# Kernel tuning notes

Hardware: AMD Instinct MI355X
Metric: run time of the kernel (lower is better)

## Reference

```python
import jax, jax.numpy as jnp
import numpy as np

NUM_HEADS = 16
LN_EPS = 1e-5


def _rope(x):
    """lucidrains RotaryEmbedding(dim_per_head // 2): rotate only the first
    Dh//2 channels with interleaved pairs; pass the rest through.
    x: (B, H, S, Dh)"""
    S, D = x.shape[-2], x.shape[-1]
    rot = D // 2
    inv_freq = 1.0 / (10000.0 ** (jnp.arange(0, rot, 2, dtype=jnp.float32) / rot))  # (rot//2,)
    ang = jnp.arange(S, dtype=jnp.float32)[:, None] * inv_freq[None, :]             # (S, rot//2)
    ang = jnp.repeat(ang, 2, axis=-1)                                               # (S, rot)
    cos, sin = jnp.cos(ang), jnp.sin(ang)
    xr, xp = x[..., :rot], x[..., rot:]
    x1, x2 = xr[..., 0::2], xr[..., 1::2]
    rot_half = jnp.stack((-x2, x1), axis=-1).reshape(xr.shape)  # interleaved (-x2, x1)
    xr = xr * cos + rot_half * sin
    return jnp.concatenate([xr, xp], axis=-1)


def setup_inputs() -> dict:
    key = jax.random.key(0)
    k1, k2, k3 = jax.random.split(key, 3)
    B, S, D = 4, 2048, 2048
    X = jax.random.normal(k1, (B, S, D), dtype=jnp.float32)
    ln_w = jnp.ones((D,), dtype=jnp.float32)
    ln_b = jnp.zeros((D,), dtype=jnp.float32)
    W_in = jax.random.normal(k2, (D, 3 * D), dtype=jnp.float32) * 0.02
    W_out = jax.random.normal(k3, (D, D), dtype=jnp.float32) * 0.02
    return {"X": X, "ln_w": ln_w, "ln_b": ln_b, "W_in": W_in, "W_out": W_out}


def reference(X, ln_w, ln_b, W_in, W_out):
    B, S, D = X.shape
    H = NUM_HEADS
    Dh = D // H
    # pre-norm (LayerNorm)
    mu = jnp.mean(X, axis=-1, keepdims=True)
    var = jnp.mean(jnp.square(X - mu), axis=-1, keepdims=True)
    Xn = (X - mu) * jax.lax.rsqrt(var + LN_EPS) * ln_w + ln_b
    # fused QKV projection
    qkv = jnp.einsum('bsd,df->bsf', Xn, W_in)            # (B, S, 3D)
    Q, K, V = jnp.split(qkv, 3, axis=-1)
    Q = Q.reshape(B, S, H, Dh).transpose(0, 2, 1, 3)     # (B, H, S, Dh)
    K = K.reshape(B, S, H, Dh).transpose(0, 2, 1, 3)
    V = V.reshape(B, S, H, Dh).transpose(0, 2, 1, 3)
    Q, K = _rope(Q), _rope(K)
    scores = jnp.einsum('bhqd,bhkd->bhqk', Q, K) / jnp.sqrt(jnp.float32(Dh))
    probs = jax.nn.softmax(scores, axis=-1)              # acausal: no mask
    ctx = jnp.einsum('bhqk,bhkd->bhqd', probs, V)
    ctx = ctx.transpose(0, 2, 1, 3).reshape(B, S, D)
    out = jnp.einsum('bsd,df->bsf', ctx, W_out)
    return out + X
```

## Files before the change

### kernel.cpp

```cpp
#include <hip/hip_runtime.h>
#include <hip/hip_bf16.h>
#include <cstddef>

#define B_ 4
#define S_ 2048
#define D_ 2048
#define H_ 16
#define DH_ 128
#define QKS_ 4096

typedef __attribute__((ext_vector_type(8))) short bfrag8;
typedef __attribute__((ext_vector_type(4))) float ffrag4;
typedef __attribute__((ext_vector_type(4))) int ifrag4;

typedef const __attribute__((address_space(1))) void* gptr1;
typedef __attribute__((address_space(3))) void* lptr3;
#define GL16(g, l) __builtin_amdgcn_global_load_lds((gptr1)(g), (lptr3)(l), 16, 0, 0)
#define LDSU(p) ((unsigned)(unsigned long long)(lptr3)(p))

#define BARRIER() { asm volatile("" ::: "memory"); __builtin_amdgcn_s_barrier(); asm volatile("" ::: "memory"); }
#define VMW8() asm volatile("s_waitcnt vmcnt(8)" ::: "memory")
#define VMW6() asm volatile("s_waitcnt vmcnt(6)" ::: "memory")
#define VMW4() asm volatile("s_waitcnt vmcnt(4)" ::: "memory")
#define VMW0() asm volatile("s_waitcnt vmcnt(0)" ::: "memory")
#define LGKM(n) { asm volatile("s_waitcnt lgkmcnt(" #n ")" ::: "memory"); __builtin_amdgcn_sched_barrier(0); }

__device__ __forceinline__ bfrag8 DSR128(unsigned a) {
  ifrag4 r;
  asm volatile("ds_read_b128 %0, %1" : "=v"(r) : "v"(a));
  return __builtin_bit_cast(bfrag8, r);
}

__device__ __forceinline__ short f2bf(float f) {
  unsigned u = __float_as_uint(f);
  u = (u + 0x7FFFu + ((u >> 16) & 1u)) >> 16;
  return (short)u;
}
__device__ __forceinline__ float bf2f(short s) {
  return __uint_as_float(((unsigned)(unsigned short)s) << 16);
}
__device__ __forceinline__ unsigned cvtpk(float lo, float hi) {
  unsigned r;
  asm("v_cvt_pk_bf16_f32 %0, %1, %2" : "=v"(r) : "v"(lo), "v"(hi));
  return r;
}

__global__ __launch_bounds__(256) void rope_tab_kernel(float2* __restrict__ tab) {
  int idx = blockIdx.x * 256 + threadIdx.x;
  int s = idx >> 5, p = idx & 31;
  float invf = exp2f(-(float)p * (13.287712379549449f / 32.0f));
  float sn, cs;
  sincosf((float)s * invf, &sn, &cs);
  tab[idx] = make_float2(cs, sn);
}

__global__ __launch_bounds__(256) void ln_kernel(const float* __restrict__ X,
    const float* __restrict__ w, const float* __restrict__ bta,
    short* __restrict__ Xn) {
  int row = blockIdx.x;
  int tid = threadIdx.x;
  const float* xr = X + (size_t)row * D_;
  float x[8];
  float4 v0 = *(const float4*)(xr + tid * 4);
  float4 v1 = *(const float4*)(xr + 1024 + tid * 4);
  x[0] = v0.x; x[1] = v0.y; x[2] = v0.z; x[3] = v0.w;
  x[4] = v1.x; x[5] = v1.y; x[6] = v1.z; x[7] = v1.w;
  float sum = 0.f, ssq = 0.f;
#pragma unroll
  for (int i = 0; i < 8; i++) { sum += x[i]; ssq += x[i] * x[i]; }
#pragma unroll
  for (int off = 1; off < 64; off <<= 1) {
    sum += __shfl_xor(sum, off, 64);
    ssq += __shfl_xor(ssq, off, 64);
  }
  __shared__ float s1[4], s2[4];
  int wave = tid >> 6;
  if ((tid & 63) == 0) { s1[wave] = sum; s2[wave] = ssq; }
  __syncthreads();
  sum = s1[0] + s1[1] + s1[2] + s1[3];
  ssq = s2[0] + s2[1] + s2[2] + s2[3];
  float mu = sum * (1.0f / D_);
  float var = ssq * (1.0f / D_) - mu * mu;
  float rs = rsqrtf(var + 1e-5f);
  short* orow = Xn + (size_t)row * D_;
#pragma unroll
  for (int i = 0; i < 8; i++) {
    int col = (i < 4) ? (tid * 4 + i) : (1024 + tid * 4 + (i - 4));
    float xn = (x[i] - mu) * rs * w[col] + bta[col];
    orow[col] = f2bf(xn);
  }
}

__global__ __launch_bounds__(256) void transpose_cvt(const float* __restrict__ W,
    short* __restrict__ WT, int R, int C) {
  __shared__ float t[32][33];
  int tx = threadIdx.x, ty = threadIdx.y;
  int c0 = blockIdx.x * 32, r0 = blockIdx.y * 32;
#pragma unroll
  for (int i = 0; i < 4; i++)
    t[ty + i * 8][tx] = W[(size_t)(r0 + ty + i * 8) * C + c0 + tx];
  __syncthreads();
#pragma unroll
  for (int i = 0; i < 4; i++)
    WT[(size_t)(c0 + ty + i * 8) * R + r0 + tx] = f2bf(t[tx][ty + i * 8]);
}

template<int EPI>
__global__ __launch_bounds__(512, 2) void gemm_bt(const short* __restrict__ A,
    const short* __restrict__ Bt, short* __restrict__ Cb, short* __restrict__ Vt,
    const float2* __restrict__ tab, float* __restrict__ Cf,
    const float* __restrict__ resid, int M, int N, int K) {
  __shared__ __align__(16) short lA[2][2][256][32];
  __shared__ __align__(16) short lB[2][2][256][32];
  int tid = threadIdx.x;
  int wave = tid >> 6, lane = tid & 63;
  int m16 = lane & 15, quad = lane >> 4;
  int wm = (wave >> 2) * 128, wn = (wave & 3) * 64;

  int bid = blockIdx.x;
  int q = bid & 7, c = bid >> 3;
  int xb = c >> 2;
  int yb = (q << 2) | (c & 3);
  int m0 = yb * 256, n0 = xb * 256;

  const ffrag4 fzero = {0.f, 0.f, 0.f, 0.f};
  ffrag4 acc[8][4];
#pragma unroll
  for (int i = 0; i < 8; i++)
#pragma unroll
    for (int j = 0; j < 4; j++) acc[i][j] = fzero;

  int r0_ = tid >> 2;
  int csw = ((tid & 3) ^ ((r0_ >> 1) & 3)) << 3;
  const short* gA0 = A + (size_t)(m0 + r0_) * K + csw;
  const short* gA1 = A + (size_t)(m0 + r0_ + 128) * K + csw;
  const short* gB0 = Bt + (size_t)(n0 + r0_) * K + csw;
  const short* gB1 = Bt + (size_t)(n0 + r0_ + 128) * K + csw;
  int ldW = wave << 10;

#define STG(g0, g1, larr, kt, h, d) { \
    const short* s0_ = (g0) + ((size_t)(kt) << 6) + ((h) << 5); \
    const short* s1_ = (g1) + ((size_t)(kt) << 6) + ((h) << 5); \
    char* dst_ = (char*)(larr) + (((d) << 15) | ((h) << 14)) + ldW; \
    GL16(s0_, dst_); \
    GL16(s1_, dst_ + 8192); }

  unsigned offA[8], offB[4];
#pragma unroll
  for (int mi = 0; mi < 8; mi++) {
    int ra = wm + mi * 16 + m16;
    offA[mi] = (unsigned)(ra * 64 + ((quad ^ ((ra >> 1) & 3)) << 4));
  }
#pragma unroll
  for (int ni = 0; ni < 4; ni++) {
    int rb = wn + ni * 16 + m16;
    offB[ni] = (unsigned)(rb * 64 + ((quad ^ ((rb >> 1) & 3)) << 4));
  }
  unsigned aLds = LDSU(&lA[0][0][0][0]);
  unsigned bLds = LDSU(&lB[0][0][0][0]);

  bfrag8 afA[4], afB[4], bfA[4], bfB[4];

#define MF16(AF, BF, BASE) { \
    __builtin_amdgcn_s_setprio(1); \
    _Pragma("unroll") \
    for (int mi_ = 0; mi_ < 4; mi_++) \
      _Pragma("unroll") \
      for (int ni_ = 0; ni_ < 4; ni_++) \
        acc[(BASE) + mi_][ni_] = __builtin_amdgcn_mfma_f32_16x16x32_bf16( \
            AF[mi_], BF[ni_], acc[(BASE) + mi_][ni_], 0, 0, 0); \
    __builtin_amdgcn_s_setprio(0); }

#define KTILE(T, S1, S2) { \
    const int cur_ = (T) & 1, nxt_ = cur_ ^ 1; \
    const unsigned h0_ = (unsigned)(cur_ << 15); \
    const unsigned h1_ = h0_ | 16384u; \
    const unsigned g0_ = (unsigned)(nxt_ << 15); \
     \
    BARRIER(); \
    afB[0] = DSR128(aLds + h0_ + offA[4]); \
    afB[1] = DSR128(aLds + h0_ + offA[5]); \
    afB[2] = DSR128(aLds + h0_ + offA[6]); \
    afB[3] = DSR128(aLds + h0_ + offA[7]); \
    if (S1) STG(gA0, gA1, lA, (T) + 1, 1, nxt_); \
    LGKM(4); \
    MF16(afA, bfA, 0); \
    if (S1) { VMW6(); } else { VMW0(); } \
     \
    BARRIER(); \
    bfB[0] = DSR128(bLds + h1_ + offB[0]); \
    bfB[1] = DSR128(bLds + h1_ + offB[1]); \
    bfB[2] = DSR128(bLds + h1_ + offB[2]); \
    bfB[3] = DSR128(bLds + h1_ + offB[3]); \
    afA[0] = DSR128(aLds + h1_ + offA[0]); \
    afA[1] = DSR128(aLds + h1_ + offA[1]); \
    afA[2] = DSR128(aLds + h1_ + offA[2]); \
    afA[3] = DSR128(aLds + h1_ + offA[3]); \
    if (S1) STG(gB0, gB1, lB, (T) + 1, 1, nxt_); \
    LGKM(8); \
    MF16(afB, bfA, 4); \
     \
    BARRIER(); \
    afB[0] = DSR128(aLds + h1_ + offA[4]); \
    afB[1] = DSR128(aLds + h1_ + offA[5]); \
    afB[2] = DSR128(aLds + h1_ + offA[6]); \
    afB[3] = DSR128(aLds + h1_ + offA[7]); \
    if (S2) STG(gA0, gA1, lA, (T) + 2, 0, cur_); \
    LGKM(4); \
    MF16(afA, bfB, 0); \
    if (S2) { VMW6(); } else if (S1) { VMW4(); } \
     \
    BARRIER(); \
    if (S1) { \
      bfA[0] = DSR128(bLds + g0_ + offB[0]); \
      bfA[1] = DSR128(bLds + g0_ + offB[1]); \
      bfA[2] = DSR128(bLds + g0_ + offB[2]); \
      bfA[3] = DSR128(bLds + g0_ + offB[3]); \
      afA[0] = DSR128(aLds + g0_ + offA[0]); \
      afA[1] = DSR128(aLds + g0_ + offA[1]); \
      afA[2] = DSR128(aLds + g0_ + offA[2]); \
      afA[3] = DSR128(aLds + g0_ + offA[3]); \
    } \
    if (S2) STG(gB0, gB1, lB, (T) + 2, 0, cur_); \
    if (S1) { LGKM(8); } else { LGKM(0); } \
    MF16(afB, bfB, 4); \
  }

  STG(gA0, gA1, lA, 0, 0, 0); STG(gB0, gB1, lB, 0, 0, 0);
  STG(gA0, gA1, lA, 0, 1, 0); STG(gB0, gB1, lB, 0, 1, 0);
  STG(gA0, gA1, lA, 1, 0, 1); STG(gB0, gB1, lB, 1, 0, 1);
  VMW8();
  BARRIER();
  bfA[0] = DSR128(bLds + offB[0]);
  bfA[1] = DSR128(bLds + offB[1]);
  bfA[2] = DSR128(bLds + offB[2]);
  bfA[3] = DSR128(bLds + offB[3]);
  afA[0] = DSR128(aLds + offA[0]);
  afA[1] = DSR128(aLds + offA[1]);
  afA[2] = DSR128(aLds + offA[2]);
  afA[3] = DSR128(aLds + offA[3]);

  int nK = K >> 6;
  for (int t = 0; t < nK - 2; ++t) KTILE(t, 1, 1);
  KTILE(nK - 2, 1, 0);
  KTILE(nK - 1, 0, 0);
#undef KTILE
#undef MF16
#undef STG

#pragma unroll
  for (int mi = 0; mi < 8; mi++) {
    int rowb = m0 + wm + mi * 16 + quad * 4;
#pragma unroll
    for (int ni = 0; ni < 4; ni++) {
      int col = n0 + wn + ni * 16 + m16;
      if (EPI == 1) {
#pragma unroll
        for (int r = 0; r < 4; r++) {
          size_t idx = (size_t)(rowb + r) * N + col;
          Cf[idx] = acc[mi][ni][r] + resid[idx];
        }
      } else if (n0 >= 4096) {
        int d = col - 4096;
        short4 pk;
        pk.x = f2bf(acc[mi][ni][0]);
        pk.y = f2bf(acc[mi][ni][1]);
        pk.z = f2bf(acc[mi][ni][2]);
        pk.w = f2bf(acc[mi][ni][3]);
        *(short4*)(Vt + ((size_t)((rowb >> 11) * H_ + (d >> 7)) * DH_ + (d & 127)) * S_ +
                   (rowb & (S_ - 1))) = pk;
      } else if ((col & 127) < 64) {
        int p = (col & 127) >> 1;
        float sgn = (col & 1) ? 1.0f : -1.0f;
#pragma unroll
        for (int r = 0; r < 4; r++) {
          float own = acc[mi][ni][r];
          float prt = __shfl_xor(own, 1, 64);
          float2 cssn = tab[((rowb + r) & (S_ - 1)) * 32 + p];
          Cb[(size_t)(rowb + r) * QKS_ + col] = f2bf(own * cssn.x + sgn * prt * cssn.y);
        }
      } else {
#pragma unroll
        for (int r = 0; r < 4; r++)
          Cb[(size_t)(rowb + r) * QKS_ + col] = f2bf(acc[mi][ni][r]);
      }
    }
  }
}

__global__ __launch_bounds__(512) void attn_kernel(const short* __restrict__ qkv,
    const short* __restrict__ Vt, short* __restrict__ ctx) {
  __shared__ __align__(16) short lK[2][64 * 128];
  __shared__ __align__(16) short lV[2][128 * 64];
  int tid = threadIdx.x;
  int wave = tid >> 6, lane = tid & 63;
  int m16 = lane & 15, quad = lane >> 4;
  int bid = blockIdx.x;
  int xcd = bid & 7, c = bid >> 3;
  int bh = ((c & 7) << 3) | xcd;
  int qchunk = c >> 3;
  int b = bh >> 4, h = bh & 15;
  int qbase = qchunk * 256 + wave * 32;

  const float qscale = 1.4426950408889634f * 0.08838834764831845f;
  bfrag8 qf[2][4];
#pragma unroll
  for (int qb = 0; qb < 2; qb++)
#pragma unroll
    for (int kc = 0; kc < 4; kc++) {
      bfrag8 q = *(const bfrag8*)(qkv +
          (size_t)(b * S_ + qbase + qb * 16 + m16) * QKS_ + h * DH_ + kc * 32 + quad * 8);
#pragma unroll
      for (int j = 0; j < 8; j++) q[j] = f2bf(bf2f(q[j]) * qscale);
      qf[qb][kc] = q;
    }

  const ffrag4 fzero = {0.f, 0.f, 0.f, 0.f};
  ffrag4 oacc[2][8];
#pragma unroll
  for (int qb = 0; qb < 2; qb++)
#pragma unroll
    for (int nd = 0; nd < 8; nd++) oacc[qb][nd] = fzero;
  float lpart[2] = {0.f, 0.f};

  int krow = lane >> 4;
  int kcb = lane & 15;
  int vrow = lane >> 3;
  int vcb = lane & 7;

  {
#pragma unroll
    for (int i = 0; i < 2; i++) {
      int c2 = wave + i * 8;
      int r = c2 * 4 + krow;
      int sb = kcb ^ (r & 15);
      GL16(qkv + (size_t)(b * S_ + r) * QKS_ + D_ + h * DH_ + sb * 8, &lK[0][c2 * 512]);
    }
#pragma unroll
    for (int i = 0; i < 2; i++) {
      int c2 = wave + i * 8;
      int r = c2 * 8 + vrow;
      int sb = vcb ^ (r & 7);
      GL16(Vt + (size_t)(bh * DH_ + r) * S_ + sb * 8, &lV[0][c2 * 512]);
    }
  }
  __syncthreads();

  for (int kt = 0; kt < 32; kt++) {
    int cur = kt & 1;
    if (kt < 31) {
      int sk0 = (kt + 1) * 64;
      int nb = cur ^ 1;
#pragma unroll
      for (int i = 0; i < 2; i++) {
        int c2 = wave + i * 8;
        int r = c2 * 4 + krow;
        int sb = kcb ^ (r & 15);
        GL16(qkv + (size_t)(b * S_ + sk0 + r) * QKS_ + D_ + h * DH_ + sb * 8, &lK[nb][c2 * 512]);
      }
#pragma unroll
      for (int i = 0; i < 2; i++) {
        int c2 = wave + i * 8;
        int r = c2 * 8 + vrow;
        int sb = vcb ^ (r & 7);
        GL16(Vt + (size_t)(bh * DH_ + r) * S_ + sk0 + sb * 8, &lV[nb][c2 * 512]);
      }
    }

    const short* kb = &lK[cur][0];
    const short* vb = &lV[cur][0];

    ffrag4 sacc[2][4];
#pragma unroll
    for (int qb = 0; qb < 2; qb++)
#pragma unroll
      for (int ntk = 0; ntk < 4; ntk++) sacc[qb][ntk] = fzero;
    __builtin_amdgcn_s_setprio(1);
#pragma unroll
    for (int ntk = 0; ntk < 4; ntk++)
#pragma unroll
      for (int kc = 0; kc < 4; kc++) {
        bfrag8 kf = *(const bfrag8*)(kb + (ntk * 16 + m16) * 128 +
                                     (((kc * 4 + quad) ^ m16) << 3));
        sacc[0][ntk] = __builtin_amdgcn_mfma_f32_16x16x32_bf16(kf, qf[0][kc], sacc[0][ntk], 0, 0, 0);
        sacc[1][ntk] = __builtin_amdgcn_mfma_f32_16x16x32_bf16(kf, qf[1][kc], sacc[1][ntk], 0, 0, 0);
      }
    __builtin_amdgcn_s_setprio(0);

    bfrag8 pA[2][2];
#pragma unroll
    for (int qb = 0; qb < 2; qb++) {
      unsigned Xp[4][2];
      float ls = 0.f;
#pragma unroll
      for (int ntk = 0; ntk < 4; ntk++) {
        float e0 = exp2f(sacc[qb][ntk][0]);
        float e1 = exp2f(sacc[qb][ntk][1]);
        float e2 = exp2f(sacc[qb][ntk][2]);
        float e3 = exp2f(sacc[qb][ntk][3]);
        ls += (e0 + e1) + (e2 + e3);
        Xp[ntk][0] = cvtpk(e0, e1);
        Xp[ntk][1] = cvtpk(e2, e3);
      }
      lpart[qb] += ls;
#pragma unroll
      for (int kc = 0; kc < 2; kc++) {
        unsigned x0 = Xp[2 * kc][0], x1 = Xp[2 * kc][1];
        unsigned y0 = Xp[2 * kc + 1][0], y1 = Xp[2 * kc + 1][1];
        asm("v_permlane32_swap_b32 %0, %1" : "+v"(x0), "+v"(y0));
        asm("v_permlane16_swap_b32 %0, %1" : "+v"(x0), "+v"(y0));
        asm("v_permlane32_swap_b32 %0, %1" : "+v"(x1), "+v"(y1));
        asm("v_permlane16_swap_b32 %0, %1" : "+v"(x1), "+v"(y1));
        union { int4 i4; bfrag8 b8; } u;
        u.i4 = (int4){(int)x0, (int)x1, (int)y0, (int)y1};
        pA[qb][kc] = u.b8;
      }
    }

    __builtin_amdgcn_s_setprio(1);
#pragma unroll
    for (int kc = 0; kc < 2; kc++)
#pragma unroll
      for (int nd = 0; nd < 8; nd++) {
        bfrag8 vf = *(const bfrag8*)(vb + (nd * 16 + m16) * 64 +
                                     (((kc * 4 + quad) ^ (m16 & 7)) << 3));
        oacc[0][nd] = __builtin_amdgcn_mfma_f32_16x16x32_bf16(pA[0][kc], vf, oacc[0][nd], 0, 0, 0);
        oacc[1][nd] = __builtin_amdgcn_mfma_f32_16x16x32_bf16(pA[1][kc], vf, oacc[1][nd], 0, 0, 0);
      }
    __builtin_amdgcn_s_setprio(0);

    __syncthreads();
  }

#pragma unroll
  for (int qb = 0; qb < 2; qb++) {
    lpart[qb] += __shfl_xor(lpart[qb], 16, 64);
    lpart[qb] += __shfl_xor(lpart[qb], 32, 64);
  }
#pragma unroll
  for (int qb = 0; qb < 2; qb++) {
    float inv[4];
#pragma unroll
    for (int r = 0; r < 4; r++) inv[r] = 1.0f / __shfl(lpart[qb], quad * 4 + r, 64);
#pragma unroll
    for (int nd = 0; nd < 8; nd++)
#pragma unroll
      for (int r = 0; r < 4; r++) {
        int row = qbase + qb * 16 + quad * 4 + r;
        int col = h * DH_ + nd * 16 + m16;
        ctx[(size_t)(b * S_ + row) * D_ + col] = f2bf(oacc[qb][nd][r] * inv[r]);
      }
  }
}

extern "C" void kernel_launch(void* const* d_in, const int* in_sizes, int n_in,
                              void* d_out, int out_size, void* d_ws, size_t ws_size,
                              hipStream_t stream) {
  const float* X    = (const float*)d_in[0];
  const float* lnw  = (const float*)d_in[1];
  const float* lnb  = (const float*)d_in[2];
  const float* Win  = (const float*)d_in[3];
  const float* Wout = (const float*)d_in[4];
  float* out = (float*)d_out;
  char* ws = (char*)d_ws;
  short*  Xn    = (short*)(ws + 0);
  short*  WinT  = (short*)(ws + 33554432);
  short*  WoutT = (short*)(ws + 58720256);
  short*  qkv   = (short*)(ws + 67108864);
  short*  Vt    = (short*)(ws + 134217728);
  short*  ctx   = (short*)(ws + 167772160);
  float2* tab   = (float2*)(ws + 201326592);

  rope_tab_kernel<<<256, 256, 0, stream>>>(tab);
  transpose_cvt<<<dim3(192, 64), dim3(32, 8), 0, stream>>>(Win, WinT, 2048, 6144);
  transpose_cvt<<<dim3(64, 64), dim3(32, 8), 0, stream>>>(Wout, WoutT, 2048, 2048);
  ln_kernel<<<8192, 256, 0, stream>>>(X, lnw, lnb, Xn);
  gemm_bt<0><<<768, 512, 0, stream>>>(Xn, WinT, qkv, Vt, tab, nullptr, nullptr, 8192, 6144, 2048);
  attn_kernel<<<512, 512, 0, stream>>>(qkv, Vt, ctx);
  gemm_bt<1><<<256, 512, 0, stream>>>(ctx, WoutT, nullptr, nullptr, nullptr, out, X, 8192, 2048, 2048);
}
```

Before: 635.6 us.

## Shrink attention blocks to 256 threads and precompute K/V load pointers

The attention kernel now launches 1024 blocks of 4 waves, each handling 128 queries instead of 256, and each wave loads four K/V chunks per tile. Per-lane global pointers for K and V are computed once and advanced by a fixed stride each tile, removing the repeated index arithmetic. Smaller blocks aim for finer scheduling granularity. In exchange, K/V tiles are reloaded by twice as many blocks, and fewer waves per CU may be resident because LDS per block is unchanged.

After: 615.1 us. -3.2%, faster.

```diff
diff --git a/kernel.cpp b/kernel.cpp
--- a/kernel.cpp
+++ b/kernel.cpp
@@ -288,7 +288,7 @@
   }
 }
 
-__global__ __launch_bounds__(512) void attn_kernel(const short* __restrict__ qkv,
+__global__ __launch_bounds__(256) void attn_kernel(const short* __restrict__ qkv,
     const short* __restrict__ Vt, short* __restrict__ ctx) {
   __shared__ __align__(16) short lK[2][64 * 128];
   __shared__ __align__(16) short lV[2][128 * 64];
@@ -300,7 +300,7 @@
   int bh = ((c & 7) << 3) | xcd;
   int qchunk = c >> 3;
   int b = bh >> 4, h = bh & 15;
-  int qbase = qchunk * 256 + wave * 32;
+  int qbase = qchunk * 128 + wave * 32;
 
   const float qscale = 1.4426950408889634f * 0.08838834764831845f;
   bfrag8 qf[2][4];
@@ -328,42 +328,39 @@
   int vrow = lane >> 3;
   int vcb = lane & 7;
 
-  {
-#pragma unroll
-    for (int i = 0; i < 2; i++) {
-      int c2 = wave + i * 8;
-      int r = c2 * 4 + krow;
-      int sb = kcb ^ (r & 15);
-      GL16(qkv + (size_t)(b * S_ + r) * QKS_ + D_ + h * DH_ + sb * 8, &lK[0][c2 * 512]);
-    }
-#pragma unroll
-    for (int i = 0; i < 2; i++) {
-      int c2 = wave + i * 8;
-      int r = c2 * 8 + vrow;
-      int sb = vcb ^ (r & 7);
-      GL16(Vt + (size_t)(bh * DH_ + r) * S_ + sb * 8, &lV[0][c2 * 512]);
-    }
-  }
+  const short* kp[4];
+  const short* vp[4];
+#pragma unroll
+  for (int i = 0; i < 4; i++) {
+    int c2 = wave + i * 4;
+    int rK = c2 * 4 + krow;
+    int sbK = kcb ^ (rK & 15);
+    kp[i] = qkv + (size_t)(b * S_ + rK) * QKS_ + D_ + h * DH_ + sbK * 8;
+    int rV = c2 * 8 + vrow;
+    int sbV = vcb ^ (rV & 7);
+    vp[i] = Vt + (size_t)(bh * DH_ + rV) * S_ + sbV * 8;
+  }
+  const size_t KSTEP = (size_t)64 * QKS_;
+
+#pragma unroll
+  for (int i = 0; i < 4; i++) GL16(kp[i], &lK[0][(wave + i * 4) * 512]);
+#pragma unroll
+  for (int i = 0; i < 4; i++) GL16(vp[i], &lV[0][(wave + i * 4) * 512]);
   __syncthreads();
 
   for (int kt = 0; kt < 32; kt++) {
     int cur = kt & 1;
     if (kt < 31) {
-      int sk0 = (kt + 1) * 64;
       int nb = cur ^ 1;
 #pragma unroll
-      for (int i = 0; i < 2; i++) {
-        int c2 = wave + i * 8;
-        int r = c2 * 4 + krow;
-        int sb = kcb ^ (r & 15);
-        GL16(qkv + (size_t)(b * S_ + sk0 + r) * QKS_ + D_ + h * DH_ + sb * 8, &lK[nb][c2 * 512]);
-      }
-#pragma unroll
-      for (int i = 0; i < 2; i++) {
-        int c2 = wave + i * 8;
-        int r = c2 * 8 + vrow;
-        int sb = vcb ^ (r & 7);
-        GL16(Vt + (size_t)(bh * DH_ + r) * S_ + sk0 + sb * 8, &lV[nb][c2 * 512]);
+      for (int i = 0; i < 4; i++) {
+        kp[i] += KSTEP;
+        GL16(kp[i], &lK[nb][(wave + i * 4) * 512]);
+      }
+#pragma unroll
+      for (int i = 0; i < 4; i++) {
+        vp[i] += 64;
+        GL16(vp[i], &lV[nb][(wave + i * 4) * 512]);
       }
     }
 
@@ -476,6 +473,6 @@
   transpose_cvt<<<dim3(64, 64), dim3(32, 8), 0, stream>>>(Wout, WoutT, 2048, 2048);
   ln_kernel<<<8192, 256, 0, stream>>>(X, lnw, lnb, Xn);
   gemm_bt<0><<<768, 512, 0, stream>>>(Xn, WinT, qkv, Vt, tab, nullptr, nullptr, 8192, 6144, 2048);
-  attn_kernel<<<512, 512, 0, stream>>>(qkv, Vt, ctx);
+  attn_kernel<<<1024, 256, 0, stream>>>(qkv, Vt, ctx);
   gemm_bt<1><<<256, 512, 0, stream>>>(ctx, WoutT, nullptr, nullptr, nullptr, out, X, 8192, 2048, 2048);
 }
```
